# Optimization experiments

Hardware: AMD Instinct MI355X
Metric: run time of the kernel (lower is better)

The kernel has to match this reference:

```python
import jax, jax.numpy as jnp
import numpy as np

B, L, D, E, H = 4, 2048, 512, 8, 1024

def setup_inputs() -> dict:
    key = jax.random.key(0)
    k1, k2, k3, k4 = jax.random.split(key, 4)
    x = jax.random.normal(k1, (B, L, D), dtype=jnp.float32)
    weights = jax.random.uniform(k2, (B, L, E), dtype=jnp.float32)
    w1 = jax.random.normal(k3, (E, D, H), dtype=jnp.float32) * 0.02
    b1 = jnp.zeros((E, H), dtype=jnp.float32)
    w2 = jax.random.normal(k4, (E, H, D), dtype=jnp.float32) * 0.02
    b2 = jnp.zeros((E, D), dtype=jnp.float32)
    return {"x": x, "weights": weights, "w1": w1, "b1": b1, "w2": w2, "b2": b2}

def reference(x, weights, w1, b1, w2, b2):
    # h: [B, L, E, H]
    h = jnp.einsum('bld,edh->bleh', x, w1) + b1[None, None, :, :]
    h = jax.nn.gelu(h, approximate=False)  # torch F.gelu default is exact (erf)
    # out: [B, L, E, D]
    out = jnp.einsum('bleh,ehd->bled', h, w2) + b2[None, None, :, :]
    # weighted sum over experts -> [B, L, D]
    return jnp.einsum('bled,ble->bld', out, weights)
```

## Files before the change

### kernel.cpp

```cpp
#include <hip/hip_runtime.h>
#include <hip/hip_bf16.h>

#define DEV __device__ __forceinline__

typedef __bf16 bf16;
typedef __bf16 bf16x4 __attribute__((ext_vector_type(4)));
typedef __bf16 bf16x8 __attribute__((ext_vector_type(8)));
typedef float f32x4 __attribute__((ext_vector_type(4)));

static constexpr int Bb = 4, Ll = 2048, Dd = 512, Ee = 8, Hh = 1024;
static constexpr int Mm = Bb * Ll;
static constexpr int GKS = Ee * Hh;

DEV void gload_lds16(const void* g, void* l) {
  __builtin_amdgcn_global_load_lds(
      (const __attribute__((address_space(1))) unsigned int*)g,
      (__attribute__((address_space(3))) unsigned int*)l, 16, 0, 0);
}

DEV float gelu_fast(float h) {
  const float k = 0.7978845608028654f * 2.0f * 1.4426950408889634f;
  float h2 = h * h;
  float y = h * (k + (0.044715f * k) * h2);
  float t = exp2f(y);
  return h - h * __frcp_rn(t + 1.0f);
}

__global__ void cvt_x_kernel(const float* __restrict__ in, bf16* __restrict__ out, int n4) {
  int i = blockIdx.x * blockDim.x + threadIdx.x;
  if (i < n4) {
    float4 v = ((const float4*)in)[i];
    bf16x4 o = {(bf16)v.x, (bf16)v.y, (bf16)v.z, (bf16)v.w};
    ((bf16x4*)out)[i] = o;
  }
}

__global__ void transpose_cvt(const float* __restrict__ in, bf16* __restrict__ out,
                              int R, int C, size_t in_es, size_t out_es, int out_rs) {
  __shared__ float tile[64][65];
  const int e = blockIdx.z;
  const float* ip = in + (size_t)e * in_es;
  bf16* op = out + (size_t)e * out_es;
  const int r0 = blockIdx.y * 64, c0 = blockIdx.x * 64;
  const int tc = threadIdx.x & 63, tr = threadIdx.x >> 6;
#pragma unroll
  for (int i = 0; i < 16; ++i) {
    const int r = tr + i * 4;
    tile[r][tc] = ip[(size_t)(r0 + r) * C + c0 + tc];
  }
  __syncthreads();
  const int wr = threadIdx.x & 63, wc0 = threadIdx.x >> 6;
#pragma unroll
  for (int i = 0; i < 16; ++i) {
    const int c = wc0 + i * 4;
    op[(size_t)(c0 + c) * out_rs + r0 + wr] = (bf16)tile[wr][c];
  }
}

template <int ARS, int BRS>
DEV void gemm128_run(const bf16* __restrict__ Ag, const bf16* __restrict__ Bg,
                     int nt_k, f32x4 (&acc)[4][4], char* lds) {
  const int t = threadIdx.x;
  const int lane = t & 63;
  const int wid = t >> 6;
  const int wm = wid >> 1, wn = wid & 1;
  const int fr = lane & 15, fg = lane >> 4;
  const int srow = t >> 2;
  const int sseg = t & 3;

  auto stage = [&](int kt, int p) {
    char* As = lds + p * 24576;
    char* Bs = lds + p * 24576 + 16384;
#pragma unroll
    for (int i = 0; i < 2; ++i) {
      const int row = i * 128 + srow;
      const int q = sseg ^ (row & 3);
      gload_lds16(Ag + (size_t)row * ARS + kt * 32 + q * 8, As + i * 8192 + wid * 1024);
    }
    {
      const int row = srow;
      const int q = sseg ^ (row & 3);
      gload_lds16(Bg + (size_t)row * BRS + kt * 32 + q * 8, Bs + wid * 1024);
    }
  };

  stage(0, 0);
  for (int kt = 0; kt < nt_k; ++kt) {
    const int p = kt & 1;
    if (kt + 1 < nt_k) {
      stage(kt + 1, p ^ 1);
      asm volatile("s_waitcnt vmcnt(3)" ::: "memory");
    } else {
      asm volatile("s_waitcnt vmcnt(0)" ::: "memory");
    }
    __builtin_amdgcn_s_barrier();
    const char* As = lds + p * 24576;
    const char* Bs = lds + p * 24576 + 16384;
    bf16x8 bfr[4], af[4];
#pragma unroll
    for (int fj = 0; fj < 4; ++fj) {
      const int row = wn * 64 + fj * 16 + fr;
      const int s = fg ^ (row & 3);
      bfr[fj] = *(const bf16x8*)(Bs + row * 64 + s * 16);
    }
#pragma unroll
    for (int fi = 0; fi < 4; ++fi) {
      const int row = wm * 64 + fi * 16 + fr;
      const int s = fg ^ (row & 3);
      af[fi] = *(const bf16x8*)(As + row * 64 + s * 16);
    }
    __builtin_amdgcn_s_setprio(1);
#pragma unroll
    for (int fi = 0; fi < 4; ++fi)
#pragma unroll
      for (int fj = 0; fj < 4; ++fj)
        acc[fi][fj] = __builtin_amdgcn_mfma_f32_16x16x32_bf16(
            bfr[fj], af[fi], acc[fi][fj], 0, 0, 0);
    __builtin_amdgcn_s_setprio(0);
    __builtin_amdgcn_s_barrier();
  }
}

__global__ __launch_bounds__(512, 4) void ffn_stage1_256(
    const bf16* __restrict__ xb, const bf16* __restrict__ w1t,
    const float* __restrict__ b1, const float* __restrict__ wts,
    bf16* __restrict__ G) {
  __shared__ __align__(16) char lds[49152];
  __shared__ float b1s[128];
  __shared__ float wls[256];
  const int mt = blockIdx.x, ct = blockIdx.y;
  const int t = threadIdx.x;
  if (t < 128) b1s[t] = b1[ct * 128 + t];
  else if (t < 384) wls[t - 128] = wts[((size_t)mt * 256 + (t - 128)) * Ee + (ct >> 3)];

  f32x4 acc[4][4] = {};
  const bf16* Ag = xb + (size_t)mt * 256 * Dd;
  const bf16* Bg = w1t + (size_t)ct * 128 * Dd;
  gemm128_run<Dd, Dd>(Ag, Bg, Dd / 32, acc, lds);

  const int lane = t & 63, wid = t >> 6;
  const int wm = wid >> 1, wn = wid & 1;
  const int fr = lane & 15, fq = lane >> 4;
  float b1v[4][4];
#pragma unroll
  for (int fj = 0; fj < 4; ++fj)
#pragma unroll
    for (int r = 0; r < 4; ++r) b1v[fj][r] = b1s[wn * 64 + fj * 16 + fq * 4 + r];
#pragma unroll
  for (int fi = 0; fi < 4; ++fi) {
    const int m = mt * 256 + wm * 64 + fi * 16 + fr;
    const float wgt = wls[wm * 64 + fi * 16 + fr];
    bf16* gp = G + (size_t)m * GKS + ct * 128 + wn * 64 + fq * 4;
#pragma unroll
    for (int fj = 0; fj < 4; ++fj) {
      bf16x4 o;
#pragma unroll
      for (int r = 0; r < 4; ++r) {
        float v = acc[fi][fj][r] + b1v[fj][r];
        o[r] = (bf16)(gelu_fast(v) * wgt);
      }
      *(bf16x4*)(gp + fj * 16) = o;
    }
  }
}

__global__ __launch_bounds__(512, 4) void ffn_stage2_256(
    const bf16* __restrict__ G, const bf16* __restrict__ w2t,
    float* __restrict__ P, int kchunk) {
  __shared__ __align__(16) char lds[49152];
  const int mt = blockIdx.x, nt = blockIdx.y, s = blockIdx.z;
  const int t = threadIdx.x;

  f32x4 acc[4][4] = {};
  const bf16* Ag = G + (size_t)mt * 256 * GKS + (size_t)s * kchunk;
  const bf16* Bg = w2t + (size_t)nt * 128 * GKS + (size_t)s * kchunk;
  gemm128_run<GKS, GKS>(Ag, Bg, kchunk / 32, acc, lds);

  float* Pp = P + (size_t)s * Mm * Dd;
  const int lane = t & 63, wid = t >> 6;
  const int wm = wid >> 1, wn = wid & 1;
  const int fr = lane & 15, fq = lane >> 4;
#pragma unroll
  for (int fi = 0; fi < 4; ++fi) {
    const size_t m = (size_t)mt * 256 + wm * 64 + fi * 16 + fr;
    float* pp = Pp + m * Dd + nt * 128 + wn * 64 + fq * 4;
#pragma unroll
    for (int fj = 0; fj < 4; ++fj) *(f32x4*)(pp + fj * 16) = acc[fi][fj];
  }
}

__global__ __launch_bounds__(256) void reduce_bias(
    const float* __restrict__ P, const float* __restrict__ wts,
    const float* __restrict__ b2, float* __restrict__ out, int S) {
  const int n4 = Mm * Dd / 4;
  int i = blockIdx.x * 256 + threadIdx.x;
  if (i >= n4) return;
  const int m = i / (Dd / 4);
  const int d0 = (i % (Dd / 4)) * 4;
  float4 a = ((const float4*)P)[i];
  for (int s = 1; s < S; ++s) {
    float4 p = ((const float4*)P)[(size_t)s * n4 + i];
    a.x += p.x; a.y += p.y; a.z += p.z; a.w += p.w;
  }
  const float* wr = wts + (size_t)m * Ee;
#pragma unroll
  for (int e = 0; e < Ee; ++e) {
    const float w = wr[e];
    float4 b = *(const float4*)(b2 + e * Dd + d0);
    a.x += w * b.x; a.y += w * b.y; a.z += w * b.z; a.w += w * b.w;
  }
  ((float4*)out)[i] = a;
}

template <int ARS, int BRS>
DEV void gemm_core(const bf16* __restrict__ Ag, const bf16* __restrict__ Bg,
                   int ksteps, f32x4 (&acc)[4][4], bf16* As, bf16* Bs) {
  const int t = threadIdx.x;
  const int lane = t & 63;
  const int w = t >> 6;
  const int srow = t >> 3;
  const int sseg = t & 7;
  const int wr = w >> 1, wc = w & 1;
  const int fr = lane & 15;
  const int fg = lane >> 4;
  for (int s = 0; s < ksteps; ++s) {
    __syncthreads();
#pragma unroll
    for (int i = 0; i < 4; ++i) {
      const int row = i * 32 + srow;
      const int q = sseg ^ (row & 7);
      gload_lds16(Ag + (size_t)row * ARS + s * 64 + q * 8,
                  (char*)As + i * 4096 + w * 1024);
      gload_lds16(Bg + (size_t)row * BRS + s * 64 + q * 8,
                  (char*)Bs + i * 4096 + w * 1024);
    }
    __syncthreads();
#pragma unroll
    for (int kk = 0; kk < 2; ++kk) {
      bf16x8 af[4], bfr[4];
#pragma unroll
      for (int mi = 0; mi < 4; ++mi) {
        const int row = wr * 64 + mi * 16 + fr;
        const int q = (kk * 4 + fg) ^ (row & 7);
        af[mi] = *(const bf16x8*)((const char*)As + row * 128 + q * 16);
      }
#pragma unroll
      for (int ni = 0; ni < 4; ++ni) {
        const int row = wc * 64 + ni * 16 + fr;
        const int q = (kk * 4 + fg) ^ (row & 7);
        bfr[ni] = *(const bf16x8*)((const char*)Bs + row * 128 + q * 16);
      }
#pragma unroll
      for (int mi = 0; mi < 4; ++mi)
#pragma unroll
        for (int ni = 0; ni < 4; ++ni)
          acc[mi][ni] = __builtin_amdgcn_mfma_f32_16x16x32_bf16(
              af[mi], bfr[ni], acc[mi][ni], 0, 0, 0);
    }
  }
}

__global__ __launch_bounds__(256) void ffn_stage1_t(
    const bf16* __restrict__ xb, const bf16* __restrict__ w1t,
    const float* __restrict__ b1, const float* __restrict__ wts,
    bf16* __restrict__ G) {
  __shared__ __align__(16) bf16 As[128 * 64];
  __shared__ __align__(16) bf16 Bs[128 * 64];
  __shared__ float b1s[128];
  __shared__ float wls[128];
  const int mt = blockIdx.x, ht = blockIdx.y, e = blockIdx.z;
  const int t = threadIdx.x;
  if (t < 128) b1s[t] = b1[e * Hh + ht * 128 + t];
  else wls[t - 128] = wts[((size_t)mt * 128 + (t - 128)) * Ee + e];
  f32x4 acc[4][4] = {};
  const bf16* Ag = xb + (size_t)mt * 128 * Dd;
  const bf16* Bg = w1t + ((size_t)e * Hh + (size_t)ht * 128) * Dd;
  gemm_core<Dd, Dd>(Ag, Bg, Dd / 64, acc, As, Bs);
  const int lane = t & 63, w = t >> 6;
  const int wr = w >> 1, wc = w & 1, fr = lane & 15, fq = lane >> 4;
  float bcol[4];
#pragma unroll
  for (int ni = 0; ni < 4; ++ni) bcol[ni] = b1s[wc * 64 + ni * 16 + fr];
  bf16* gp = G + ((size_t)mt * 128 + wr * 64 + fq * 4) * GKS
               + (size_t)e * Hh + ht * 128 + wc * 64 + fr;
#pragma unroll
  for (int mi = 0; mi < 4; ++mi)
#pragma unroll
    for (int r = 0; r < 4; ++r) {
      const float wgt = wls[wr * 64 + mi * 16 + fq * 4 + r];
#pragma unroll
      for (int ni = 0; ni < 4; ++ni) {
        float v = acc[mi][ni][r] + bcol[ni];
        gp[(size_t)(mi * 16 + r) * GKS + ni * 16] = (bf16)(gelu_fast(v) * wgt);
      }
    }
}

__global__ __launch_bounds__(256) void ffn_stage2_partial(
    const bf16* __restrict__ G, const bf16* __restrict__ w2t,
    float* __restrict__ P, int kchunk) {
  __shared__ __align__(16) bf16 As[128 * 64];
  __shared__ __align__(16) bf16 Bs[128 * 64];
  const int mt = blockIdx.x, nt = blockIdx.y, s = blockIdx.z;
  f32x4 acc[4][4] = {};
  const bf16* Ag = G + (size_t)mt * 128 * GKS + (size_t)s * kchunk;
  const bf16* Bg = w2t + (size_t)nt * 128 * GKS + (size_t)s * kchunk;
  gemm_core<GKS, GKS>(Ag, Bg, kchunk / 64, acc, As, Bs);
  float* Pp = P + (size_t)s * Mm * Dd;
  const int t = threadIdx.x;
  const int lane = t & 63, w = t >> 6;
  const int wr = w >> 1, wc = w & 1, fr = lane & 15, fq = lane >> 4;
#pragma unroll
  for (int mi = 0; mi < 4; ++mi)
#pragma unroll
    for (int r = 0; r < 4; ++r) {
      const size_t m = (size_t)mt * 128 + wr * 64 + mi * 16 + fq * 4 + r;
#pragma unroll
      for (int ni = 0; ni < 4; ++ni) {
        const int d = nt * 128 + wc * 64 + ni * 16 + fr;
        Pp[m * Dd + d] = acc[mi][ni][r];
      }
    }
}

extern "C" void kernel_launch(void* const* d_in, const int* in_sizes, int n_in,
                              void* d_out, int out_size, void* d_ws, size_t ws_size,
                              hipStream_t stream) {
  const float* x   = (const float*)d_in[0];
  const float* wts = (const float*)d_in[1];
  const float* w1  = (const float*)d_in[2];
  const float* b1  = (const float*)d_in[3];
  const float* w2  = (const float*)d_in[4];
  const float* b2  = (const float*)d_in[5];
  float* out = (float*)d_out;

  char* ws = (char*)d_ws;
  size_t off = 0;
  bf16* xb  = (bf16*)(ws + off); off += (size_t)Mm * Dd * 2;
  bf16* w1t = (bf16*)(ws + off); off += (size_t)Ee * Hh * Dd * 2;
  bf16* w2t = (bf16*)(ws + off); off += (size_t)Dd * Ee * Hh * 2;

  const size_t gfull = (size_t)Mm * Ee * Hh * 2;
  const size_t psz   = (size_t)Mm * Dd * 4;

  cvt_x_kernel<<<(Mm * Dd / 4 + 255) / 256, 256, 0, stream>>>(x, xb, Mm * Dd / 4);
  transpose_cvt<<<dim3(Hh / 64, Dd / 64, Ee), 256, 0, stream>>>(
      w1, w1t, Dd, Hh, (size_t)Dd * Hh, (size_t)Hh * Dd, Dd);
  transpose_cvt<<<dim3(Dd / 64, Hh / 64, Ee), 256, 0, stream>>>(
      w2, w2t, Hh, Dd, (size_t)Hh * Dd, (size_t)Hh, Ee * Hh);

  if (ws_size >= off + gfull + 4 * psz) {
    bf16* G = (bf16*)(ws + off);
    float* P = (float*)(ws + off + gfull);
    ffn_stage1_256<<<dim3(Mm / 256, GKS / 128), 512, 0, stream>>>(
        xb, w1t, b1, wts, G);
    ffn_stage2_256<<<dim3(Mm / 256, Dd / 128, 4), 512, 0, stream>>>(
        G, w2t, P, GKS / 4);
    reduce_bias<<<(Mm * Dd / 4 + 255) / 256, 256, 0, stream>>>(P, wts, b2, out, 4);
  } else if (ws_size >= off + gfull + 2 * psz) {
    bf16* G = (bf16*)(ws + off);
    float* P = (float*)(ws + off + gfull);
    ffn_stage1_t<<<dim3(Mm / 128, Hh / 128, Ee), 256, 0, stream>>>(
        xb, w1t, b1, wts, G);
    ffn_stage2_partial<<<dim3(Mm / 128, Dd / 128, 2), 256, 0, stream>>>(
        G, w2t, P, GKS / 2);
    reduce_bias<<<(Mm * Dd / 4 + 255) / 256, 256, 0, stream>>>(P, wts, b2, out, 2);
  }
}
```

Baseline: 227.3 us.

## Triple-buffer GEMM LDS staging and simplify swizzle index computation

Moves the shared GEMM mainloop from double to triple buffering in LDS. Loads are issued two k-tiles ahead and waited on with a deeper vmcnt, so more global-memory latency is hidden. The XOR swizzle is recomputed once per thread instead of per row inside the loop. LDS per block grows from 48KB to 72KB, which can cut how many blocks fit per CU and reduce occupancy.

```diff
diff --git a/kernel.cpp b/kernel.cpp
--- a/kernel.cpp
+++ b/kernel.cpp
@@ -66,48 +66,44 @@
   const int wm = wid >> 1, wn = wid & 1;
   const int fr = lane & 15, fg = lane >> 4;
   const int srow = t >> 2;
-  const int sseg = t & 3;
+  const int sq = (t & 3) ^ ((t >> 4) & 3);
+  const int rsl = fg ^ (fr >> 2);
 
   auto stage = [&](int kt, int p) {
     char* As = lds + p * 24576;
     char* Bs = lds + p * 24576 + 16384;
 #pragma unroll
-    for (int i = 0; i < 2; ++i) {
-      const int row = i * 128 + srow;
-      const int q = sseg ^ (row & 3);
-      gload_lds16(Ag + (size_t)row * ARS + kt * 32 + q * 8, As + i * 8192 + wid * 1024);
-    }
-    {
-      const int row = srow;
-      const int q = sseg ^ (row & 3);
-      gload_lds16(Bg + (size_t)row * BRS + kt * 32 + q * 8, Bs + wid * 1024);
-    }
+    for (int i = 0; i < 2; ++i)
+      gload_lds16(Ag + (size_t)(i * 128 + srow) * ARS + kt * 32 + sq * 8,
+                  As + i * 8192 + wid * 1024);
+    gload_lds16(Bg + (size_t)srow * BRS + kt * 32 + sq * 8, Bs + wid * 1024);
   };
 
   stage(0, 0);
+  if (nt_k > 1) stage(1, 1);
+  int cur = 0, stg = 2;
   for (int kt = 0; kt < nt_k; ++kt) {
-    const int p = kt & 1;
-    if (kt + 1 < nt_k) {
-      stage(kt + 1, p ^ 1);
+    if (kt + 2 < nt_k) {
+      stage(kt + 2, stg);
+      asm volatile("s_waitcnt vmcnt(6)" ::: "memory");
+    } else if (kt + 1 < nt_k) {
       asm volatile("s_waitcnt vmcnt(3)" ::: "memory");
     } else {
       asm volatile("s_waitcnt vmcnt(0)" ::: "memory");
     }
     __builtin_amdgcn_s_barrier();
-    const char* As = lds + p * 24576;
-    const char* Bs = lds + p * 24576 + 16384;
+    const char* As = lds + cur * 24576;
+    const char* Bs = lds + cur * 24576 + 16384;
     bf16x8 bfr[4], af[4];
 #pragma unroll
     for (int fj = 0; fj < 4; ++fj) {
       const int row = wn * 64 + fj * 16 + fr;
-      const int s = fg ^ (row & 3);
-      bfr[fj] = *(const bf16x8*)(Bs + row * 64 + s * 16);
+      bfr[fj] = *(const bf16x8*)(Bs + row * 64 + rsl * 16);
     }
 #pragma unroll
     for (int fi = 0; fi < 4; ++fi) {
       const int row = wm * 64 + fi * 16 + fr;
-      const int s = fg ^ (row & 3);
-      af[fi] = *(const bf16x8*)(As + row * 64 + s * 16);
+      af[fi] = *(const bf16x8*)(As + row * 64 + rsl * 16);
     }
     __builtin_amdgcn_s_setprio(1);
 #pragma unroll
@@ -118,6 +114,8 @@
             bfr[fj], af[fi], acc[fi][fj], 0, 0, 0);
     __builtin_amdgcn_s_setprio(0);
     __builtin_amdgcn_s_barrier();
+    cur = cur == 2 ? 0 : cur + 1;
+    stg = stg == 2 ? 0 : stg + 1;
   }
 }
 
@@ -125,7 +123,7 @@
     const bf16* __restrict__ xb, const bf16* __restrict__ w1t,
     const float* __restrict__ b1, const float* __restrict__ wts,
     bf16* __restrict__ G) {
-  __shared__ __align__(16) char lds[49152];
+  __shared__ __align__(16) char lds[73728];
   __shared__ float b1s[128];
   __shared__ float wls[256];
   const int mt = blockIdx.x, ct = blockIdx.y;
@@ -167,7 +165,7 @@
 __global__ __launch_bounds__(512, 4) void ffn_stage2_256(
     const bf16* __restrict__ G, const bf16* __restrict__ w2t,
     float* __restrict__ P, int kchunk) {
-  __shared__ __align__(16) char lds[49152];
+  __shared__ __align__(16) char lds[73728];
   const int mt = blockIdx.x, nt = blockIdx.y, s = blockIdx.z;
   const int t = threadIdx.x;
 
```

Result: no change. 226.8 us (-0.2%).
